# Kernel tuning notes

Hardware: AMD Instinct MI355X
Metric: run time of the kernel (lower is better)

## Reference

```python
import jax, jax.numpy as jnp
import numpy as np

DIM = 768
N_HEADS = 12
HEAD_DIM = DIM // N_HEADS
B, S = 2, 4096


def setup_inputs() -> dict:
    key = jax.random.key(0)
    k_x, k_wqkv, k_bqkv, k_wout, k_bout = jax.random.split(key, 5)
    scale_in = 1.0 / np.sqrt(DIM)
    return {
        "x": jax.random.normal(k_x, (B, S, DIM), dtype=jnp.float32),
        "Wqkv": jax.random.normal(k_wqkv, (DIM, 3 * DIM), dtype=jnp.float32) * scale_in,
        "bqkv": jax.random.normal(k_bqkv, (3 * DIM,), dtype=jnp.float32) * 0.02,
        "Wout": jax.random.normal(k_wout, (DIM, DIM), dtype=jnp.float32) * scale_in,
        "bout": jax.random.normal(k_bout, (DIM,), dtype=jnp.float32) * 0.02,
    }


def reference(x, Wqkv, bqkv, Wout, bout):
    b, s, d = x.shape
    qkv = (x @ Wqkv + bqkv).reshape(b, s, 3, N_HEADS, HEAD_DIM)
    qkv = jnp.transpose(qkv, (2, 0, 3, 1, 4))  # [3, B, H, S, hd]
    q, k, v = qkv[0], qkv[1], qkv[2]
    scale = HEAD_DIM ** -0.5
    attn = jnp.einsum('bhqd,bhkd->bhqk', q, k) * scale  # [B, H, S, S]
    causal_mask = jnp.triu(jnp.ones((s, s), dtype=bool), k=1)
    attn = jnp.where(causal_mask[None, None], -jnp.inf, attn)
    attn = jax.nn.softmax(attn, axis=-1)
    out = jnp.einsum('bhqk,bhkd->bhqd', attn, v)  # [B, H, S, hd]
    out = jnp.transpose(out, (0, 2, 1, 3)).reshape(b, s, d)
    return out @ Wout + bout
```

## Files before the change

### kernel.cpp

```cpp
#include <hip/hip_runtime.h>
#include <hip/hip_bf16.h>
#include <math.h>

#define DIM 768
#define NH 12
#define HD 64
#define BATCH 2
#define SEQ 4096
#define MTOT (BATCH * SEQ)

#define QSCALE 0.1803368801111244f

typedef unsigned short u16;
typedef __bf16 bf16x8 __attribute__((ext_vector_type(8)));
typedef float  f32x4  __attribute__((ext_vector_type(4)));
typedef unsigned short u16x4 __attribute__((ext_vector_type(4)));
typedef unsigned short u16x8 __attribute__((ext_vector_type(8)));

__device__ inline u16 f2bf(float f) {
    unsigned u = __builtin_bit_cast(unsigned, f);
    u += 0x7fffu + ((u >> 16) & 1u);
    return (u16)(u >> 16);
}

__device__ inline f32x4 mfma16(bf16x8 a, bf16x8 b, f32x4 c) {
    return __builtin_amdgcn_mfma_f32_16x16x32_bf16(a, b, c, 0, 0, 0);
}

__device__ inline void gl2lds16(const u16* g, u16* l) {
    __builtin_amdgcn_global_load_lds(
        (const __attribute__((address_space(1))) void*)g,
        (__attribute__((address_space(3))) void*)l,
        16, 0, 0);
}

__global__ __launch_bounds__(256)
void cvt_bf16(const float* __restrict__ src, u16* __restrict__ dst, int n8)
{
    int i = blockIdx.x * 256 + threadIdx.x;
    if (i >= n8) return;
    float4 a = ((const float4*)src)[i * 2];
    float4 b = ((const float4*)src)[i * 2 + 1];
    u16x8 o;
    o[0] = f2bf(a.x); o[1] = f2bf(a.y); o[2] = f2bf(a.z); o[3] = f2bf(a.w);
    o[4] = f2bf(b.x); o[5] = f2bf(b.y); o[6] = f2bf(b.z); o[7] = f2bf(b.w);
    ((u16x8*)dst)[i] = o;
}

__global__ __launch_bounds__(256)
void transpose_to_bf16(const float* __restrict__ src, u16* __restrict__ dst,
                       int R, int C)
{
    __shared__ float tile[32][33];
    const int c0 = blockIdx.x * 32, r0 = blockIdx.y * 32;
    const int tx = threadIdx.x & 31, ty = threadIdx.x >> 5;
#pragma unroll
    for (int i = 0; i < 4; ++i) {
        int row = ty * 4 + i;
        tile[row][tx] = src[(size_t)(r0 + row) * C + c0 + tx];
    }
    __syncthreads();
#pragma unroll
    for (int i = 0; i < 4; ++i) {
        int crow = ty * 4 + i;
        dst[(size_t)(c0 + crow) * R + r0 + tx] = f2bf(tile[tx][crow]);
    }
}

__device__ inline void gemm_lds_mainloop(const u16* __restrict__ Ag,
                                         const u16* __restrict__ Bg,
                                         int m0, int n0, int w, int lane,
                                         u16 (*As)[64 * 64], u16 (*Bs)[64 * 64],
                                         f32x4 acc[4][4])
{
    const int quad = lane >> 4, lc = lane & 15;
    const int wm = (w & 1) * 64, wn = (w >> 1) * 64;
    const int drow = lane >> 3;
    const int dp   = lane & 7;

#pragma unroll
    for (int mi = 0; mi < 4; ++mi)
#pragma unroll
        for (int nj = 0; nj < 4; ++nj)
            acc[mi][nj] = f32x4{0.f, 0.f, 0.f, 0.f};

#pragma unroll
    for (int i = 0; i < 2; ++i) {
        const int r  = w * 16 + i * 8 + drow;
        const int g  = dp ^ (r & 7);
        const int tr = 2 * r + (g >> 2);
        const int kc = g & 3;
        gl2lds16(Ag + (size_t)(m0 + tr) * 768 + kc * 8, &As[0][(w * 16 + i * 8) * 64]);
        gl2lds16(Bg + (size_t)(n0 + tr) * 768 + kc * 8, &Bs[0][(w * 16 + i * 8) * 64]);
    }
    __syncthreads();

    for (int ks = 0; ks < 24; ++ks) {
        const int cur = ks & 1;

        if (ks < 23) {
            const int k0n = (ks + 1) * 32;
#pragma unroll
            for (int i = 0; i < 2; ++i) {
                const int r  = w * 16 + i * 8 + drow;
                const int g  = dp ^ (r & 7);
                const int tr = 2 * r + (g >> 2);
                const int kc = g & 3;
                gl2lds16(Ag + (size_t)(m0 + tr) * 768 + k0n + kc * 8,
                         &As[1 - cur][(w * 16 + i * 8) * 64]);
                gl2lds16(Bg + (size_t)(n0 + tr) * 768 + k0n + kc * 8,
                         &Bs[1 - cur][(w * 16 + i * 8) * 64]);
            }
        }

        bf16x8 af[4], bfr[4];
#pragma unroll
        for (int mi = 0; mi < 4; ++mi) {
            const int m = wm + mi * 16 + lc;
            const int r = m >> 1;
            const int p = (((m & 1) * 4 + quad)) ^ (r & 7);
            af[mi] = *(const bf16x8*)&As[cur][r * 64 + p * 8];
        }
#pragma unroll
        for (int nj = 0; nj < 4; ++nj) {
            const int n = wn + nj * 16 + lc;
            const int r = n >> 1;
            const int p = (((n & 1) * 4 + quad)) ^ (r & 7);
            bfr[nj] = *(const bf16x8*)&Bs[cur][r * 64 + p * 8];
        }

#pragma unroll
        for (int mi = 0; mi < 4; ++mi)
#pragma unroll
            for (int nj = 0; nj < 4; ++nj)
                acc[mi][nj] = mfma16(af[mi], bfr[nj], acc[mi][nj]);

        __syncthreads();
    }
}

__global__ __launch_bounds__(256)
void gemm_qkv_mfma(const u16* __restrict__ A, const u16* __restrict__ Bt,
                   const float* __restrict__ bias,
                   u16* __restrict__ Qb, u16* __restrict__ Kb, u16* __restrict__ Vt)
{
    __shared__ u16 As[2][64 * 64];
    __shared__ u16 Bs[2][64 * 64];
    const int m0 = blockIdx.x * 128;
    const int n0 = blockIdx.y * 128;
    const int t = threadIdx.x;
    const int w = t >> 6, lane = t & 63;
    const int quad = lane >> 4, lc = lane & 15;
    const int wm = (w & 1) * 64, wn = (w >> 1) * 64;

    f32x4 acc[4][4];
    gemm_lds_mainloop(A, Bt, m0, n0, w, lane, As, Bs, acc);

    const int b  = m0 >> 12;
    const int s0 = (m0 & 4095) + wm;
    const int nbase = n0 + wn;
    const int three = nbase / 768;
    const int rem   = nbase - three * 768;
    const int h     = rem >> 6;
    const int bh    = b * NH + h;

    if (three < 2) {
        u16* dst = (three == 0) ? Qb : Kb;
        const float qs = (three == 0) ? QSCALE : 1.0f;
#pragma unroll
        for (int nj = 0; nj < 4; ++nj) {
            const float bi = bias[nbase + nj * 16 + lc];
            const int d = nj * 16 + lc;
#pragma unroll
            for (int mi = 0; mi < 4; ++mi) {
                const int s = s0 + mi * 16 + quad * 4;
#pragma unroll
                for (int r = 0; r < 4; ++r)
                    dst[((size_t)bh * SEQ + s + r) * HD + d] = f2bf((acc[mi][nj][r] + bi) * qs);
            }
        }
    } else {
#pragma unroll
        for (int nj = 0; nj < 4; ++nj) {
            const float bi = bias[nbase + nj * 16 + lc];
            const int d = nj * 16 + lc;
            const size_t rowb = ((size_t)bh * HD + d) * SEQ;
#pragma unroll
            for (int mi = 0; mi < 4; ++mi) {
                const int s = s0 + mi * 16 + quad * 4;
                u16x4 wv;
#pragma unroll
                for (int r = 0; r < 4; ++r) wv[r] = f2bf(acc[mi][nj][r] + bi);
                *(u16x4*)&Vt[rowb + s] = wv;
            }
        }
    }
}

__global__ __launch_bounds__(256)
void gemm_out_mfma(const u16* __restrict__ A, const u16* __restrict__ Bt,
                   const float* __restrict__ bias, float* __restrict__ C)
{
    __shared__ u16 As[2][64 * 64];
    __shared__ u16 Bs[2][64 * 64];
    const int m0 = blockIdx.x * 128;
    const int n0 = blockIdx.y * 128;
    const int t = threadIdx.x;
    const int w = t >> 6, lane = t & 63;
    const int quad = lane >> 4, lc = lane & 15;
    const int wm = (w & 1) * 64, wn = (w >> 1) * 64;

    f32x4 acc[4][4];
    gemm_lds_mainloop(A, Bt, m0, n0, w, lane, As, Bs, acc);

#pragma unroll
    for (int nj = 0; nj < 4; ++nj) {
        const int col = n0 + wn + nj * 16 + lc;
        const float bi = bias[col];
#pragma unroll
        for (int mi = 0; mi < 4; ++mi) {
            const int row = m0 + wm + mi * 16 + quad * 4;
#pragma unroll
            for (int r = 0; r < 4; ++r)
                C[(size_t)(row + r) * 768 + col] = acc[mi][nj][r] + bi;
        }
    }
}

__global__ __launch_bounds__(256)
void flash_attn(const u16* __restrict__ Qg, const u16* __restrict__ Kg,
                const u16* __restrict__ Vtg, u16* __restrict__ Og)
{
    const int pair = blockIdx.x;
    const int bh   = blockIdx.y;
    const int b    = bh / NH, h = bh % NH;
    const int t    = threadIdx.x;
    const int w    = t >> 6;
    const int lane = t & 63;
    const int quad = lane >> 4;
    const int lc   = lane & 15;
    const int drow = lane >> 3;
    const int dp   = lane & 7;

    __shared__ u16 Ks[2][64 * 64];
    __shared__ u16 Vs[2][64 * 64];
    __shared__ u16 Pl[4][16][72];

    const u16* Qp = Qg  + (size_t)bh * SEQ * HD;
    const u16* Kp = Kg  + (size_t)bh * SEQ * HD;
    const u16* Vp = Vtg + (size_t)bh * HD * SEQ;

#pragma unroll 1
    for (int half = 0; half < 2; ++half) {
        const int qt    = half ? (63 - pair) : pair;
        const int qrow0 = qt * 64 + w * 16;

        const bf16x8 qa0 = *(const bf16x8*)&Qp[(size_t)(qrow0 + lc) * HD + quad * 8];
        const bf16x8 qa1 = *(const bf16x8*)&Qp[(size_t)(qrow0 + lc) * HD + 32 + quad * 8];

        f32x4 o[4];
        float l_r[4];
#pragma unroll
        for (int n = 0; n < 4; ++n) o[n] = f32x4{0.f, 0.f, 0.f, 0.f};
#pragma unroll
        for (int r = 0; r < 4; ++r) l_r[r] = 0.f;

        {
#pragma unroll
            for (int i = 0; i < 2; ++i) {
                const int r0  = w * 16 + i * 8;
                const int row = r0 + drow;
                const int gc  = dp ^ (row & 7);
                gl2lds16(Kp + (size_t)row * HD + gc * 8, &Ks[0][r0 * 64]);
                gl2lds16(Vp + (size_t)row * SEQ + gc * 8, &Vs[0][r0 * 64]);
            }
        }
        __syncthreads();

        for (int tk = 0; tk <= qt; ++tk) {
            const int kb  = tk * 64;
            const int cur = tk & 1;

            if (tk < qt) {
                const int kbn = kb + 64;
#pragma unroll
                for (int i = 0; i < 2; ++i) {
                    const int r0  = w * 16 + i * 8;
                    const int row = r0 + drow;
                    const int gc  = dp ^ (row & 7);
                    gl2lds16(Kp + (size_t)(kbn + row) * HD + gc * 8,
                             &Ks[1 - cur][r0 * 64]);
                    gl2lds16(Vp + (size_t)row * SEQ + kbn + gc * 8,
                             &Vs[1 - cur][r0 * 64]);
                }
            }

            f32x4 sacc[4];
#pragma unroll
            for (int n = 0; n < 4; ++n) sacc[n] = f32x4{0.f, 0.f, 0.f, 0.f};
#pragma unroll
            for (int n = 0; n < 4; ++n) {
                const int row = n * 16 + lc;
                const int sw  = row & 7;
                bf16x8 k0 = *(const bf16x8*)&Ks[cur][row * 64 + (quad ^ sw) * 8];
                bf16x8 k1 = *(const bf16x8*)&Ks[cur][row * 64 + ((quad + 4) ^ sw) * 8];
                sacc[n] = mfma16(qa0, k0, sacc[n]);
                sacc[n] = mfma16(qa1, k1, sacc[n]);
            }

            if (tk == qt) {
#pragma unroll
                for (int n = 0; n < 4; ++n) {
                    const int key = kb + n * 16 + lc;
#pragma unroll
                    for (int r = 0; r < 4; ++r)
                        if (key > qrow0 + quad * 4 + r) sacc[n][r] = -1e30f;
                }
            }

#pragma unroll
            for (int n = 0; n < 4; ++n) {
#pragma unroll
                for (int r = 0; r < 4; ++r) {
                    float p = __builtin_amdgcn_exp2f(sacc[n][r]);
                    l_r[r] += p;
                    Pl[w][quad * 4 + r][n * 16 + lc] = f2bf(p);
                }
            }

            const bf16x8 pa0 = *(const bf16x8*)&Pl[w][lc][quad * 8];
            const bf16x8 pa1 = *(const bf16x8*)&Pl[w][lc][32 + quad * 8];
#pragma unroll
            for (int n = 0; n < 4; ++n) {
                const int row = n * 16 + lc;
                const int sw  = row & 7;
                bf16x8 v0 = *(const bf16x8*)&Vs[cur][row * 64 + (quad ^ sw) * 8];
                bf16x8 v1 = *(const bf16x8*)&Vs[cur][row * 64 + ((quad + 4) ^ sw) * 8];
                o[n] = mfma16(pa0, v0, o[n]);
                o[n] = mfma16(pa1, v1, o[n]);
            }

            __syncthreads();
        }

#pragma unroll
        for (int r = 0; r < 4; ++r) {
            float rs = l_r[r];
            rs += __shfl_xor(rs, 1);
            rs += __shfl_xor(rs, 2);
            rs += __shfl_xor(rs, 4);
            rs += __shfl_xor(rs, 8);
            const float inv = 1.0f / rs;
            const int   q   = qrow0 + quad * 4 + r;
            const size_t base = ((size_t)(b * SEQ + q)) * DIM + h * HD + lc;
            Og[base +  0] = f2bf(o[0][r] * inv);
            Og[base + 16] = f2bf(o[1][r] * inv);
            Og[base + 32] = f2bf(o[2][r] * inv);
            Og[base + 48] = f2bf(o[3][r] * inv);
        }
    }
}

extern "C" void kernel_launch(void* const* d_in, const int* in_sizes, int n_in,
                              void* d_out, int out_size, void* d_ws, size_t ws_size,
                              hipStream_t stream)
{
    const float* x    = (const float*)d_in[0];
    const float* Wqkv = (const float*)d_in[1];
    const float* bqkv = (const float*)d_in[2];
    const float* Wout = (const float*)d_in[3];
    const float* bout = (const float*)d_in[4];
    float* out = (float*)d_out;

    const size_t NX  = (size_t)MTOT * DIM;
    const size_t NWQ = (size_t)DIM * 3 * DIM;
    const size_t NWO = (size_t)DIM * DIM;
    u16* p   = (u16*)d_ws;
    u16* Xb  = p;              p += NX;
    u16* Wqt = p;              p += NWQ;
    u16* Wot = p;              p += NWO;
    u16* Qb  = p;              p += NX;
    u16* Kb  = p;              p += NX;
    u16* Vt  = p;              p += NX;
    u16* Ao  = p;

    cvt_bf16<<<(int)(NX / 8 + 255) / 256, 256, 0, stream>>>(x, Xb, (int)(NX / 8));
    transpose_to_bf16<<<dim3(2304 / 32, 768 / 32), 256, 0, stream>>>(Wqkv, Wqt, 768, 2304);
    transpose_to_bf16<<<dim3(768 / 32, 768 / 32), 256, 0, stream>>>(Wout, Wot, 768, 768);

    gemm_qkv_mfma<<<dim3(MTOT / 128, 2304 / 128), 256, 0, stream>>>(Xb, Wqt, bqkv, Qb, Kb, Vt);
    flash_attn<<<dim3(32, BATCH * NH), 256, 0, stream>>>(Qb, Kb, Vt, Ao);
    gemm_out_mfma<<<dim3(MTOT / 128, 768 / 128), 256, 0, stream>>>(Ao, Wot, bout, out);
}
```

Baseline: 266.1 us.

## Split flash-attention warps 2x2 over query and key halves with LDS reduction

Reorganizes the attention block so each of four waves handles 32 query rows against half of the 64-key tile, reusing each K and V fragment across two query subtiles. Partial outputs and row sums from the two key-half waves are combined through shared memory at the end. The grid is swapped so heads vary fastest and the heavier query tile runs first. This is meant to cut LDS fragment reads per MFMA, at the cost of an extra reduction step and more synchronisation.

```diff
diff --git a/kernel.cpp b/kernel.cpp
--- a/kernel.cpp
+++ b/kernel.cpp
@@ -231,11 +231,13 @@
 void flash_attn(const u16* __restrict__ Qg, const u16* __restrict__ Kg,
                 const u16* __restrict__ Vtg, u16* __restrict__ Og)
 {
-    const int pair = blockIdx.x;
-    const int bh   = blockIdx.y;
+    const int bh   = blockIdx.x;
+    const int pair = blockIdx.y;
     const int b    = bh / NH, h = bh % NH;
     const int t    = threadIdx.x;
     const int w    = t >> 6;
+    const int wq   = w >> 1;
+    const int wk   = w & 1;
     const int lane = t & 63;
     const int quad = lane >> 4;
     const int lc   = lane & 15;
@@ -244,36 +246,45 @@
 
     __shared__ u16 Ks[2][64 * 64];
     __shared__ u16 Vs[2][64 * 64];
-    __shared__ u16 Pl[4][16][72];
+    __shared__ u16 Pl[4][32][40];
+    __shared__ float Lx[2][32];
 
     const u16* Qp = Qg  + (size_t)bh * SEQ * HD;
     const u16* Kp = Kg  + (size_t)bh * SEQ * HD;
     const u16* Vp = Vtg + (size_t)bh * HD * SEQ;
+    float* Vscr = (float*)&Vs[0][0];
 
 #pragma unroll 1
     for (int half = 0; half < 2; ++half) {
-        const int qt    = half ? (63 - pair) : pair;
-        const int qrow0 = qt * 64 + w * 16;
-
-        const bf16x8 qa0 = *(const bf16x8*)&Qp[(size_t)(qrow0 + lc) * HD + quad * 8];
-        const bf16x8 qa1 = *(const bf16x8*)&Qp[(size_t)(qrow0 + lc) * HD + 32 + quad * 8];
-
-        f32x4 o[4];
-        float l_r[4];
-#pragma unroll
-        for (int n = 0; n < 4; ++n) o[n] = f32x4{0.f, 0.f, 0.f, 0.f};
-#pragma unroll
-        for (int r = 0; r < 4; ++r) l_r[r] = 0.f;
-
-        {
-#pragma unroll
-            for (int i = 0; i < 2; ++i) {
-                const int r0  = w * 16 + i * 8;
-                const int row = r0 + drow;
-                const int gc  = dp ^ (row & 7);
-                gl2lds16(Kp + (size_t)row * HD + gc * 8, &Ks[0][r0 * 64]);
-                gl2lds16(Vp + (size_t)row * SEQ + gc * 8, &Vs[0][r0 * 64]);
-            }
+        const int qt    = half ? pair : (63 - pair);
+        const int qrow0 = qt * 64 + wq * 32;
+
+        bf16x8 qa[2][2];
+#pragma unroll
+        for (int mi = 0; mi < 2; ++mi)
+#pragma unroll
+            for (int hk = 0; hk < 2; ++hk)
+                qa[mi][hk] = *(const bf16x8*)
+                    &Qp[(size_t)(qrow0 + mi * 16 + lc) * HD + hk * 32 + quad * 8];
+
+        f32x4 o[2][4];
+        float l_r[2][4];
+#pragma unroll
+        for (int mi = 0; mi < 2; ++mi)
+#pragma unroll
+            for (int nd = 0; nd < 4; ++nd) o[mi][nd] = f32x4{0.f, 0.f, 0.f, 0.f};
+#pragma unroll
+        for (int mi = 0; mi < 2; ++mi)
+#pragma unroll
+            for (int r = 0; r < 4; ++r) l_r[mi][r] = 0.f;
+
+#pragma unroll
+        for (int i = 0; i < 2; ++i) {
+            const int r0  = w * 16 + i * 8;
+            const int row = r0 + drow;
+            const int gc  = dp ^ (row & 7);
+            gl2lds16(Kp + (size_t)row * HD + gc * 8, &Ks[0][r0 * 64]);
+            gl2lds16(Vp + (size_t)row * SEQ + gc * 8, &Vs[0][r0 * 64]);
         }
         __syncthreads();
 
@@ -295,69 +306,118 @@
                 }
             }
 
-            f32x4 sacc[4];
-#pragma unroll
-            for (int n = 0; n < 4; ++n) sacc[n] = f32x4{0.f, 0.f, 0.f, 0.f};
-#pragma unroll
-            for (int n = 0; n < 4; ++n) {
-                const int row = n * 16 + lc;
+            bf16x8 kf[2][2];
+#pragma unroll
+            for (int nj = 0; nj < 2; ++nj) {
+                const int row = wk * 32 + nj * 16 + lc;
                 const int sw  = row & 7;
-                bf16x8 k0 = *(const bf16x8*)&Ks[cur][row * 64 + (quad ^ sw) * 8];
-                bf16x8 k1 = *(const bf16x8*)&Ks[cur][row * 64 + ((quad + 4) ^ sw) * 8];
-                sacc[n] = mfma16(qa0, k0, sacc[n]);
-                sacc[n] = mfma16(qa1, k1, sacc[n]);
-            }
+#pragma unroll
+                for (int hk = 0; hk < 2; ++hk)
+                    kf[nj][hk] = *(const bf16x8*)
+                        &Ks[cur][row * 64 + ((quad + 4 * hk) ^ sw) * 8];
+            }
+
+            f32x4 sacc[2][2];
+#pragma unroll
+            for (int mi = 0; mi < 2; ++mi)
+#pragma unroll
+                for (int nj = 0; nj < 2; ++nj) {
+                    f32x4 s = f32x4{0.f, 0.f, 0.f, 0.f};
+                    s = mfma16(qa[mi][0], kf[nj][0], s);
+                    s = mfma16(qa[mi][1], kf[nj][1], s);
+                    sacc[mi][nj] = s;
+                }
 
             if (tk == qt) {
 #pragma unroll
-                for (int n = 0; n < 4; ++n) {
-                    const int key = kb + n * 16 + lc;
+                for (int mi = 0; mi < 2; ++mi)
+#pragma unroll
+                    for (int nj = 0; nj < 2; ++nj) {
+                        const int key = kb + wk * 32 + nj * 16 + lc;
+                        const int qb2 = qrow0 + mi * 16 + quad * 4;
+#pragma unroll
+                        for (int r = 0; r < 4; ++r)
+                            if (key > qb2 + r) sacc[mi][nj][r] = -1e30f;
+                    }
+            }
+
+#pragma unroll
+            for (int mi = 0; mi < 2; ++mi)
+#pragma unroll
+                for (int nj = 0; nj < 2; ++nj)
+#pragma unroll
+                    for (int r = 0; r < 4; ++r) {
+                        float p = __builtin_amdgcn_exp2f(sacc[mi][nj][r]);
+                        l_r[mi][r] += p;
+                        Pl[w][mi * 16 + quad * 4 + r][nj * 16 + lc] = f2bf(p);
+                    }
+
+            bf16x8 pa[2];
+#pragma unroll
+            for (int mi = 0; mi < 2; ++mi)
+                pa[mi] = *(const bf16x8*)&Pl[w][mi * 16 + lc][quad * 8];
+#pragma unroll
+            for (int nd = 0; nd < 4; ++nd) {
+                const int row = nd * 16 + lc;
+                const int sw  = row & 7;
+                bf16x8 vf = *(const bf16x8*)
+                    &Vs[cur][row * 64 + ((wk * 4 + quad) ^ sw) * 8];
+                o[0][nd] = mfma16(pa[0], vf, o[0][nd]);
+                o[1][nd] = mfma16(pa[1], vf, o[1][nd]);
+            }
+
+            __syncthreads();
+        }
+
+#pragma unroll
+        for (int mi = 0; mi < 2; ++mi)
+#pragma unroll
+            for (int r = 0; r < 4; ++r) {
+                float rs = l_r[mi][r];
+                rs += __shfl_xor(rs, 1);
+                rs += __shfl_xor(rs, 2);
+                rs += __shfl_xor(rs, 4);
+                rs += __shfl_xor(rs, 8);
+                l_r[mi][r] = rs;
+            }
+
+        if (wk == 1) {
+#pragma unroll
+            for (int mi = 0; mi < 2; ++mi)
+#pragma unroll
+                for (int nd = 0; nd < 4; ++nd)
 #pragma unroll
                     for (int r = 0; r < 4; ++r)
-                        if (key > qrow0 + quad * 4 + r) sacc[n][r] = -1e30f;
+                        Vscr[wq * 2048 + (mi * 16 + quad * 4 + r) * 64 + nd * 16 + lc]
+                            = o[mi][nd][r];
+            if (lc == 0) {
+#pragma unroll
+                for (int mi = 0; mi < 2; ++mi)
+#pragma unroll
+                    for (int r = 0; r < 4; ++r)
+                        Lx[wq][mi * 16 + quad * 4 + r] = l_r[mi][r];
+            }
+        }
+        __syncthreads();
+        if (wk == 0) {
+#pragma unroll
+            for (int mi = 0; mi < 2; ++mi)
+#pragma unroll
+                for (int r = 0; r < 4; ++r) {
+                    const int rowl = mi * 16 + quad * 4 + r;
+                    const float lsum = l_r[mi][r] + Lx[wq][rowl];
+                    const float inv  = 1.0f / lsum;
+                    const int q = qrow0 + rowl;
+                    const size_t base = ((size_t)(b * SEQ + q)) * DIM + h * HD + lc;
+#pragma unroll
+                    for (int nd = 0; nd < 4; ++nd) {
+                        const float ov = o[mi][nd][r]
+                            + Vscr[wq * 2048 + rowl * 64 + nd * 16 + lc];
+                        Og[base + nd * 16] = f2bf(ov * inv);
+                    }
                 }
-            }
-
-#pragma unroll
-            for (int n = 0; n < 4; ++n) {
-#pragma unroll
-                for (int r = 0; r < 4; ++r) {
-                    float p = __builtin_amdgcn_exp2f(sacc[n][r]);
-                    l_r[r] += p;
-                    Pl[w][quad * 4 + r][n * 16 + lc] = f2bf(p);
-                }
-            }
-
-            const bf16x8 pa0 = *(const bf16x8*)&Pl[w][lc][quad * 8];
-            const bf16x8 pa1 = *(const bf16x8*)&Pl[w][lc][32 + quad * 8];
-#pragma unroll
-            for (int n = 0; n < 4; ++n) {
-                const int row = n * 16 + lc;
-                const int sw  = row & 7;
-                bf16x8 v0 = *(const bf16x8*)&Vs[cur][row * 64 + (quad ^ sw) * 8];
-                bf16x8 v1 = *(const bf16x8*)&Vs[cur][row * 64 + ((quad + 4) ^ sw) * 8];
-                o[n] = mfma16(pa0, v0, o[n]);
-                o[n] = mfma16(pa1, v1, o[n]);
-            }
-
-            __syncthreads();
-        }
-
-#pragma unroll
-        for (int r = 0; r < 4; ++r) {
-            float rs = l_r[r];
-            rs += __shfl_xor(rs, 1);
-            rs += __shfl_xor(rs, 2);
-            rs += __shfl_xor(rs, 4);
-            rs += __shfl_xor(rs, 8);
-            const float inv = 1.0f / rs;
-            const int   q   = qrow0 + quad * 4 + r;
-            const size_t base = ((size_t)(b * SEQ + q)) * DIM + h * HD + lc;
-            Og[base +  0] = f2bf(o[0][r] * inv);
-            Og[base + 16] = f2bf(o[1][r] * inv);
-            Og[base + 32] = f2bf(o[2][r] * inv);
-            Og[base + 48] = f2bf(o[3][r] * inv);
-        }
+        }
+        __syncthreads();
     }
 }
 
@@ -389,6 +449,6 @@
     transpose_to_bf16<<<dim3(768 / 32, 768 / 32), 256, 0, stream>>>(Wout, Wot, 768, 768);
 
     gemm_qkv_mfma<<<dim3(MTOT / 128, 2304 / 128), 256, 0, stream>>>(Xb, Wqt, bqkv, Qb, Kb, Vt);
-    flash_attn<<<dim3(32, BATCH * NH), 256, 0, stream>>>(Qb, Kb, Vt, Ao);
+    flash_attn<<<dim3(24, 32), 256, 0, stream>>>(Qb, Kb, Vt, Ao);
     gemm_out_mfma<<<dim3(MTOT / 128, 768 / 128), 256, 0, stream>>>(Ao, Wot, bout, out);
 }
```

New measurement: 251.9 us. 1.06x faster.
